# Performance work log

Hardware: AMD Instinct MI355X
Metric: run time of the kernel (lower is better)

Reference implementation:

```python
import jax, jax.numpy as jnp
import numpy as np

EPS = 1e-5  # BatchNorm eps (torch default)


def _coords():
    # coord_tensor[i] = [(i//5 - 2)/2, (i%5 - 2)/2] for 5x5 grid of 25 objects
    i = jnp.arange(25)
    return jnp.stack([(i // 5 - 2) / 2.0, (i % 5 - 2) / 2.0], axis=-1).astype(jnp.float32)


def _conv_bn(x, w, b, gamma, beta):
    # conv stride2 pad1 -> relu -> batchnorm (training-mode batch stats, as torch module default)
    y = jax.lax.conv_general_dilated(x, w, (2, 2), ((1, 1), (1, 1)),
                                     dimension_numbers=('NCHW', 'OIHW', 'NCHW'))
    y = jax.nn.relu(y + b[None, :, None, None])
    m = y.mean(axis=(0, 2, 3), keepdims=True)
    v = y.var(axis=(0, 2, 3), keepdims=True)
    return gamma[None, :, None, None] * (y - m) * jax.lax.rsqrt(v + EPS) + beta[None, :, None, None]


def setup_inputs() -> dict:
    key = jax.random.key(0)
    ks = iter(jax.random.split(key, 64))
    def rn(shape, scale=0.05):
        return jax.random.normal(next(ks), shape, jnp.float32) * scale
    B = 256
    inp = {
        'x': jax.random.normal(next(ks), (B, 3, 80, 80), jnp.float32),
        'qst': jax.random.normal(next(ks), (B, 11), jnp.float32),
    }
    for l, (ci, co) in enumerate([(3, 24), (24, 24), (24, 24), (24, 24)], 1):
        inp[f'cw{l}'] = rn((co, ci, 3, 3))
        inp[f'cb{l}'] = jnp.zeros((co,), jnp.float32)
        inp[f'bg{l}'] = jnp.ones((co,), jnp.float32)
        inp[f'bb{l}'] = jnp.zeros((co,), jnp.float32)
    for l, (di, do) in enumerate([(63, 256), (256, 256), (256, 256), (256, 256)], 1):
        inp[f'gw{l}'] = rn((di, do))
        inp[f'gb{l}'] = jnp.zeros((do,), jnp.float32)
    for l, (di, do) in enumerate([(256, 256), (256, 256), (256, 10)], 1):
        inp[f'fw{l}'] = rn((di, do))
        inp[f'fb{l}'] = jnp.zeros((do,), jnp.float32)
    return inp


def _forward(x, qst, cw1, cb1, bg1, bb1, cw2, cb2, bg2, bb2,
             cw3, cb3, bg3, bb3, cw4, cb4, bg4, bb4,
             gw1, gb1, gw2, gb2, gw3, gb3, gw4, gb4,
             fw1, fb1, fw2, fb2, fw3, fb3):
    B = x.shape[0]
    # Convolution stack: (B,3,80,80) -> (B,24,5,5)
    h = _conv_bn(x, cw1, cb1, bg1, bb1)
    h = _conv_bn(h, cw2, cb2, bg2, bb2)
    h = _conv_bn(h, cw3, cb3, bg3, bb3)
    h = _conv_bn(h, cw4, cb4, bg4, bb4)
    # Objects: (B,24,25) -> (B,25,24) -> concat coords -> (B,25,26)
    obj = h.reshape(B, 24, 25).transpose(0, 2, 1)
    obj = jnp.concatenate([obj, jnp.broadcast_to(_coords()[None], (B, 25, 2))], axis=-1)
    # Pairwise broadcast-concat: cat([x_i, x_j, qst]) with x_i[b,p,q]=obj[b,q], x_j[b,p,q]=obj[b,p]
    xi = jnp.broadcast_to(obj[:, None, :, :], (B, 25, 25, 26))
    xj = jnp.broadcast_to(obj[:, :, None, :], (B, 25, 25, 26))
    qb = jnp.broadcast_to(qst[:, None, None, :], (B, 25, 25, 11))
    pairs = jnp.concatenate([xi, xj, qb], axis=-1).reshape(B, 625, 63)
    g = jax.nn.relu(pairs @ gw1 + gb1)
    g = jax.nn.relu(g @ gw2 + gb2)
    g = jax.nn.relu(g @ gw3 + gb3)
    g = jax.nn.relu(g @ gw4 + gb4).sum(axis=1)  # (B,256)
    # f_phi (dropout treated as identity for a deterministic reference)
    f = jax.nn.relu(g @ fw1 + fb1)
    f = jax.nn.relu(f @ fw2 + fb2)
    logits = f @ fw3 + fb3
    return jax.nn.log_softmax(logits, axis=1)


def reference(x, qst, cw1, cb1, bg1, bb1, cw2, cb2, bg2, bb2,
              cw3, cb3, bg3, bb3, cw4, cb4, bg4, bb4,
              gw1, gb1, gw2, gb2, gw3, gb3, gw4, gb4,
              fw1, fb1, fw2, fb2, fw3, fb3):
    return _forward(x, qst, cw1, cb1, bg1, bb1, cw2, cb2, bg2, bb2,
                    cw3, cb3, bg3, bb3, cw4, cb4, bg4, bb4,
                    gw1, gb1, gw2, gb2, gw3, gb3, gw4, gb4,
                    fw1, fb1, fw2, fb2, fw3, fb3)
```

## Files before the change

### kernel.cpp

```cpp
#include <hip/hip_runtime.h>
#include <hip/hip_bf16.h>


typedef __attribute__((ext_vector_type(8))) short short8;
typedef __attribute__((ext_vector_type(4))) float floatx4;

__device__ __forceinline__ unsigned short f2bf(float v){
  union { float f; unsigned int u; } c; c.f = v;
  unsigned int u = c.u;
  u += 0x7FFFu + ((u >> 16) & 1u);
  return (unsigned short)(u >> 16);
}

__global__ __launch_bounds__(256) void prep_w_zero(
    const float* __restrict__ gw2, const float* __restrict__ gw3,
    const float* __restrict__ gw4, unsigned short* __restrict__ wf,
    float* __restrict__ stats)
{
  const int bid = blockIdx.x, tid = threadIdx.x;
  if (bid == 0){ for (int j = tid; j < 1536; j += 256) stats[j] = 0.f; }
  const int w = bid >> 8;
  const float* gw = (w == 0) ? gw2 : (w == 1) ? gw3 : gw4;
  const int idx = (bid & 255)*256 + tid;
  const int i = idx & 7, lane = (idx >> 3) & 63, t = (idx >> 9) & 15, kk = idx >> 13;
  const int k = kk*32 + (lane >> 4)*8 + i;
  const int c = t*16 + (lane & 15);
  wf[w*65536 + idx] = f2bf(gw[k*256 + c]);
}

template<int CI, int COG>
__global__ __launch_bounds__(256) void conv_relu_stats(
    const float* __restrict__ in,
    const float* __restrict__ stats_in, const float* __restrict__ gprev,
    const float* __restrict__ bprev, float invN,
    const float* __restrict__ cw, const float* __restrict__ cb,
    float* __restrict__ out, float* __restrict__ stats_out,
    int H, int W, int OH, int OW)
{
  const int co0 = blockIdx.y * COG;
  __shared__ float ssm[2*CI];
  __shared__ float psum[4][COG], psum2[4][COG];
  const int tid = threadIdx.x;
  if (tid < CI){
    if (stats_in){
      float S = 0.f, S2 = 0.f;
      #pragma unroll
      for (int sh = 0; sh < 8; sh++){ S += stats_in[sh*48 + tid]; S2 += stats_in[sh*48 + 24 + tid]; }
      const float mean = S*invN;
      const float var  = S2*invN - mean*mean;
      const float rs   = rsqrtf(var + 1e-5f);
      const float sc   = gprev[tid]*rs;
      ssm[tid] = sc; ssm[CI + tid] = bprev[tid] - mean*sc;
    } else { ssm[tid] = 1.f; ssm[CI + tid] = 0.f; }
  }
  __syncthreads();
  const int idx = blockIdx.x*256 + tid;
  const int ow = idx % OW; const int t2 = idx / OW;
  const int oh = t2 % OH;  const int b  = t2 / OH;
  const float* cwb = cw + co0*CI*9;
  float accv[COG];
  #pragma unroll
  for (int g = 0; g < COG; g++) accv[g] = cb[co0 + g];
  for (int ci = 0; ci < CI; ci++){
    const float* ip = in + ((long)(b*CI + ci))*H*W;
    const float sc = ssm[ci], sh2 = ssm[CI + ci];
    #pragma unroll
    for (int kh = 0; kh < 3; kh++){
      const int ih = oh*2 - 1 + kh;
      if ((unsigned)ih >= (unsigned)H) continue;
      #pragma unroll
      for (int kw = 0; kw < 3; kw++){
        const int iw = ow*2 - 1 + kw;
        if ((unsigned)iw >= (unsigned)W) continue;
        const float v = ip[ih*W + iw]*sc + sh2;
        #pragma unroll
        for (int g = 0; g < COG; g++)
          accv[g] += v * cwb[(g*CI + ci)*9 + kh*3 + kw];
      }
    }
  }
  const int wave = tid >> 6, lane = tid & 63;
  #pragma unroll
  for (int g = 0; g < COG; g++){
    const float v = fmaxf(accv[g], 0.f);
    accv[g] = v;
    out[(((long)b*24 + co0 + g)*OH + oh)*OW + ow] = v;
  }
  #pragma unroll
  for (int g = 0; g < COG; g++){
    float s = accv[g], s2 = accv[g]*accv[g];
    for (int off = 32; off; off >>= 1){ s += __shfl_down(s, off); s2 += __shfl_down(s2, off); }
    if (lane == 0){ psum[wave][g] = s; psum2[wave][g] = s2; }
  }
  __syncthreads();
  if (tid < COG){
    const float S  = psum[0][tid] + psum[1][tid] + psum[2][tid] + psum[3][tid];
    const float S2 = psum2[0][tid] + psum2[1][tid] + psum2[2][tid] + psum2[3][tid];
    const int sh = blockIdx.x & 7;
    atomicAdd(&stats_out[sh*48 + co0 + tid],      S);
    atomicAdd(&stats_out[sh*48 + 24 + co0 + tid], S2);
  }
}

__global__ __launch_bounds__(256) void build_ABQ(
    const float* __restrict__ y4, const float* __restrict__ stats4,
    const float* __restrict__ bg4, const float* __restrict__ bb4,
    const float* __restrict__ qst, const float* __restrict__ gw1,
    const float* __restrict__ gb1,
    float* __restrict__ A, float* __restrict__ Bm, float* __restrict__ Qv)
{
  const int b = blockIdx.x, tid = threadIdx.x;
  __shared__ float ssm[48];
  __shared__ float obj[25][26];
  if (tid < 24){
    float S = 0.f, S2 = 0.f;
    #pragma unroll
    for (int sh = 0; sh < 8; sh++){ S += stats4[sh*48 + tid]; S2 += stats4[sh*48 + 24 + tid]; }
    const float mean = S*(1.f/6400.f);
    const float var  = S2*(1.f/6400.f) - mean*mean;
    const float rs   = rsqrtf(var + 1e-5f);
    const float sc   = bg4[tid]*rs;
    ssm[tid] = sc; ssm[24 + tid] = bb4[tid] - mean*sc;
  }
  __syncthreads();
  for (int j = tid; j < 600; j += 256){
    const int q = j/24, c = j%24;
    obj[q][c] = ssm[c]*y4[((long)(b*24 + c))*25 + q] + ssm[24 + c];
  }
  if (tid < 50){
    const int q = tid >> 1;
    obj[q][24 + (tid & 1)] = (tid & 1) ? (float)(q%5 - 2)*0.5f : (float)(q/5 - 2)*0.5f;
  }
  __syncthreads();
  const int n = tid;
  float wa[26], wb[26];
  #pragma unroll
  for (int c = 0; c < 26; c++){ wa[c] = gw1[c*256 + n]; wb[c] = gw1[(26 + c)*256 + n]; }
  float qv = gb1[n];
  #pragma unroll
  for (int j = 0; j < 11; j++) qv += qst[b*11 + j]*gw1[(52 + j)*256 + n];
  Qv[b*256 + n] = qv;
  for (int q = 0; q < 25; q++){
    float a = 0.f, bm = 0.f;
    #pragma unroll
    for (int c = 0; c < 26; c++){ const float o = obj[q][c]; a += o*wa[c]; bm += o*wb[c]; }
    A [((long)(b*25 + q))*256 + n] = a;
    Bm[((long)(b*25 + q))*256 + n] = bm;
  }
}

__global__ __launch_bounds__(512) void g_fused(
    const float* __restrict__ A, const float* __restrict__ Bm, const float* __restrict__ Qv,
    const unsigned short* __restrict__ Wf,
    const float* __restrict__ gb2, const float* __restrict__ gb3, const float* __restrict__ gb4,
    float* __restrict__ gpart)
{
  __shared__ __align__(16) short act[128*256];
  __shared__ float scratch[512];
  const int tid = threadIdx.x;
  const int bidx = blockIdx.x;
  const int b = bidx / 5, blk = bidx % 5;
  const int rowbase = blk * 128;
  const int nrows = min(128, 625 - rowbase);
  char* actB = (char*)act;
  const int wave = tid >> 6, lane = tid & 63;
  const int lmod = lane & 15, ldiv = lane >> 4;
  const int wm = wave >> 2, wn = wave & 3;

  {
    const int r  = tid >> 2;
    const int q4 = tid & 3;
    if (r < nrows){
      const int row = rowbase + r;
      const float* ap = A  + ((long)(b*25 + row % 25))*256 + q4*4;
      const float* bp = Bm + ((long)(b*25 + row / 25))*256 + q4*4;
      const float* qp = Qv + b*256 + q4*4;
      #pragma unroll
      for (int j = 0; j < 16; j++){
        const int c = j*16;
        floatx4 av = *(const floatx4*)(ap + c);
        floatx4 bv = *(const floatx4*)(bp + c);
        floatx4 qv = *(const floatx4*)(qp + c);
        unsigned int p0 = (unsigned int)f2bf(fmaxf(av.x+bv.x+qv.x, 0.f))
                        | ((unsigned int)f2bf(fmaxf(av.y+bv.y+qv.y, 0.f)) << 16);
        unsigned int p1 = (unsigned int)f2bf(fmaxf(av.z+bv.z+qv.z, 0.f))
                        | ((unsigned int)f2bf(fmaxf(av.w+bv.w+qv.w, 0.f)) << 16);
        const int byte = (r*512 + (c + q4*4)*2) ^ ((r & 7) << 4);
        *(uint2*)(actB + byte) = make_uint2(p0, p1);
      }
    } else {
      #pragma unroll
      for (int j = 0; j < 16; j++){
        const int byte = (r*512 + (j*16 + q4*4)*2) ^ ((r & 7) << 4);
        *(uint2*)(actB + byte) = make_uint2(0u, 0u);
      }
    }
  }
  __syncthreads();

  for (int L = 0; L < 3; L++){
    floatx4 acc[4][4];
    #pragma unroll
    for (int m = 0; m < 4; m++)
      #pragma unroll
      for (int n = 0; n < 4; n++)
        acc[m][n] = (floatx4){0.f,0.f,0.f,0.f};
    const short8* wlayer = (const short8*)Wf + (long)L*8192;
    #pragma unroll
    for (int kk = 0; kk < 8; kk++){
      short8 bf[4];
      #pragma unroll
      for (int n = 0; n < 4; n++)
        bf[n] = wlayer[(kk*16 + wn*4 + n)*64 + lane];
      short8 af[4];
      #pragma unroll
      for (int m = 0; m < 4; m++){
        const int arow  = wm*64 + m*16 + lmod;
        const int abyte = (arow*512 + kk*64 + ldiv*16) ^ ((arow & 7) << 4);
        af[m] = *(const short8*)(actB + abyte);
      }
      #pragma unroll
      for (int n = 0; n < 4; n++)
        #pragma unroll
        for (int m = 0; m < 4; m++)
          acc[m][n] = __builtin_amdgcn_mfma_f32_16x16x32_bf16(af[m], bf[n], acc[m][n], 0, 0, 0);
    }

    if (L < 2){
      const float* bias = (L == 0) ? gb2 : gb3;
      __syncthreads();
      #pragma unroll
      for (int n = 0; n < 4; n++){
        const int c = (wn*4 + n)*16 + lmod;
        const float bv = bias[c];
        #pragma unroll
        for (int m = 0; m < 4; m++){
          #pragma unroll
          for (int i = 0; i < 4; i++){
            const int row = wm*64 + m*16 + ldiv*4 + i;
            const float v = fmaxf(acc[m][n][i] + bv, 0.f);
            const int byte = (row*512 + c*2) ^ ((row & 7) << 4);
            *(short*)(actB + byte) = (short)f2bf(v);
          }
        }
      }
      __syncthreads();
    } else {
      #pragma unroll
      for (int n = 0; n < 4; n++){
        const int c = (wn*4 + n)*16 + lmod;
        const float bv = gb4[c];
        float sv = 0.f;
        #pragma unroll
        for (int m = 0; m < 4; m++){
          #pragma unroll
          for (int i = 0; i < 4; i++){
            const int row = wm*64 + m*16 + ldiv*4 + i;
            const float v = fmaxf(acc[m][n][i] + bv, 0.f);
            if (row < nrows) sv += v;
          }
        }
        sv += __shfl_xor(sv, 16);
        sv += __shfl_xor(sv, 32);
        if (ldiv == 0) scratch[wm*256 + c] = sv;
      }
      __syncthreads();
      if (tid < 256) gpart[(long)bidx*256 + tid] = scratch[tid] + scratch[256 + tid];
    }
  }
}

__global__ __launch_bounds__(256) void f_phi(
    const float* __restrict__ gpart,
    const float* __restrict__ fw1, const float* __restrict__ fb1,
    const float* __restrict__ fw2, const float* __restrict__ fb2,
    const float* __restrict__ fw3, const float* __restrict__ fb3,
    float* __restrict__ out)
{
  const int b = blockIdx.x, n = threadIdx.x;
  __shared__ __align__(16) float bufA[256], bufB[256];
  __shared__ float lg[10];
  float g = 0.f;
  #pragma unroll
  for (int j = 0; j < 5; j++) g += gpart[((long)(b*5 + j))*256 + n];
  bufA[n] = g;
  __syncthreads();
  float acc = fb1[n];
  {
    const float4* pa = (const float4*)bufA;
    #pragma unroll 8
    for (int k4 = 0; k4 < 64; k4++){
      const float4 a = pa[k4];
      acc += a.x*fw1[(k4*4 + 0)*256 + n];
      acc += a.y*fw1[(k4*4 + 1)*256 + n];
      acc += a.z*fw1[(k4*4 + 2)*256 + n];
      acc += a.w*fw1[(k4*4 + 3)*256 + n];
    }
  }
  bufB[n] = fmaxf(acc, 0.f);
  __syncthreads();
  acc = fb2[n];
  {
    const float4* pb = (const float4*)bufB;
    #pragma unroll 8
    for (int k4 = 0; k4 < 64; k4++){
      const float4 a = pb[k4];
      acc += a.x*fw2[(k4*4 + 0)*256 + n];
      acc += a.y*fw2[(k4*4 + 1)*256 + n];
      acc += a.z*fw2[(k4*4 + 2)*256 + n];
      acc += a.w*fw2[(k4*4 + 3)*256 + n];
    }
  }
  __syncthreads();
  bufA[n] = fmaxf(acc, 0.f);
  __syncthreads();
  if (n < 10){
    float a3 = fb3[n];
    for (int k = 0; k < 256; k++) a3 += bufA[k]*fw3[k*10 + n];
    lg[n] = a3;
  }
  __syncthreads();
  if (n < 10){
    float m = lg[0];
    #pragma unroll
    for (int j = 1; j < 10; j++) m = fmaxf(m, lg[j]);
    float s = 0.f;
    #pragma unroll
    for (int j = 0; j < 10; j++) s += expf(lg[j] - m);
    out[b*10 + n] = lg[n] - m - logf(s);
  }
}

extern "C" void kernel_launch(void* const* d_in, const int* in_sizes, int n_in,
                              void* d_out, int out_size, void* d_ws, size_t ws_size,
                              hipStream_t stream)
{
  const float* x   = (const float*)d_in[0];
  const float* qst = (const float*)d_in[1];
  const float* cw1 = (const float*)d_in[2];
  const float* cb1 = (const float*)d_in[3];
  const float* bg1 = (const float*)d_in[4];
  const float* bb1 = (const float*)d_in[5];
  const float* cw2 = (const float*)d_in[6];
  const float* cb2 = (const float*)d_in[7];
  const float* bg2 = (const float*)d_in[8];
  const float* bb2 = (const float*)d_in[9];
  const float* cw3 = (const float*)d_in[10];
  const float* cb3 = (const float*)d_in[11];
  const float* bg3 = (const float*)d_in[12];
  const float* bb3 = (const float*)d_in[13];
  const float* cw4 = (const float*)d_in[14];
  const float* cb4 = (const float*)d_in[15];
  const float* bg4 = (const float*)d_in[16];
  const float* bb4 = (const float*)d_in[17];
  const float* gw1 = (const float*)d_in[18];
  const float* gb1 = (const float*)d_in[19];
  const float* gw2 = (const float*)d_in[20];
  const float* gb2 = (const float*)d_in[21];
  const float* gw3 = (const float*)d_in[22];
  const float* gb3 = (const float*)d_in[23];
  const float* gw4 = (const float*)d_in[24];
  const float* gb4 = (const float*)d_in[25];
  const float* fw1 = (const float*)d_in[26];
  const float* fb1 = (const float*)d_in[27];
  const float* fw2 = (const float*)d_in[28];
  const float* fb2 = (const float*)d_in[29];
  const float* fw3 = (const float*)d_in[30];
  const float* fb3 = (const float*)d_in[31];

  float* wsf    = (float*)d_ws;
  float* Qv     = wsf + 192;
  unsigned short* Wf = (unsigned short*)(wsf + 65728);
  float* stats  = wsf + 164032;
  float* y1     = wsf + 240832;
  float* Abuf   = y1;
  float* Bmbuf  = y1 + 1638400;
  float* y2     = wsf + 10071232;
  float* gpart  = y2;
  float* y3     = wsf + 12528832;
  float* y4     = wsf + 13143232;

  prep_w_zero<<<768, 256, 0, stream>>>(gw2, gw3, gw4, Wf, stats);
  conv_relu_stats<3,24><<<dim3(1600,1), 256, 0, stream>>>(x, nullptr, nullptr, nullptr, 0.f,
                                               cw1, cb1, y1, stats + 0, 80,80,40,40);
  conv_relu_stats<24,8><<<dim3(400,3), 256, 0, stream>>>(y1, stats + 0, bg1, bb1, 1.f/409600.f,
                                               cw2, cb2, y2, stats + 384, 40,40,20,20);
  conv_relu_stats<24,8><<<dim3(100,3), 256, 0, stream>>>(y2, stats + 384, bg2, bb2, 1.f/102400.f,
                                               cw3, cb3, y3, stats + 768, 20,20,10,10);
  conv_relu_stats<24,8><<<dim3(25,3), 256, 0, stream>>>(y3, stats + 768, bg3, bb3, 1.f/25600.f,
                                              cw4, cb4, y4, stats + 1152, 10,10,5,5);
  build_ABQ<<<256, 256, 0, stream>>>(y4, stats + 1152, bg4, bb4, qst, gw1, gb1,
                                     Abuf, Bmbuf, Qv);
  g_fused<<<1280, 512, 0, stream>>>(Abuf, Bmbuf, Qv, Wf, gb2, gb3, gb4, gpart);
  f_phi<<<256, 256, 0, stream>>>(gpart, fw1, fb1, fw2, fb2, fw3, fb3, (float*)d_out);
}
```

Baseline: 311.1 us.

## Fuse weight prep with conv1 and compute two outputs per thread in conv2/3

Merges the bf16 weight-swizzle kernel and the first convolution into one launch, with block ranges selecting the job, and moves the stats zeroing to a memset. Conv layers 2 and 3 now use a specialized kernel where each thread computes two adjacent output columns. The two outputs share a 5-wide input window, and their results are written as float2 stores. This cuts one kernel launch and reduces redundant input loads and index math, but adds per-thread register pressure and halves the grid size for those layers.

Measured after the change: 344.3 us. 1.11x slower.

```diff
diff --git a/kernel.cpp b/kernel.cpp
--- a/kernel.cpp
+++ b/kernel.cpp
@@ -12,20 +12,149 @@
   return (unsigned short)(u >> 16);
 }
 
-__global__ __launch_bounds__(256) void prep_w_zero(
+__global__ __launch_bounds__(256) void prep_conv1(
     const float* __restrict__ gw2, const float* __restrict__ gw3,
     const float* __restrict__ gw4, unsigned short* __restrict__ wf,
-    float* __restrict__ stats)
+    const float* __restrict__ x, const float* __restrict__ cw, const float* __restrict__ cb,
+    float* __restrict__ out, float* __restrict__ stats_out)
 {
   const int bid = blockIdx.x, tid = threadIdx.x;
-  if (bid == 0){ for (int j = tid; j < 1536; j += 256) stats[j] = 0.f; }
-  const int w = bid >> 8;
-  const float* gw = (w == 0) ? gw2 : (w == 1) ? gw3 : gw4;
-  const int idx = (bid & 255)*256 + tid;
-  const int i = idx & 7, lane = (idx >> 3) & 63, t = (idx >> 9) & 15, kk = idx >> 13;
-  const int k = kk*32 + (lane >> 4)*8 + i;
-  const int c = t*16 + (lane & 15);
-  wf[w*65536 + idx] = f2bf(gw[k*256 + c]);
+  if (bid < 768){
+    const int w = bid >> 8;
+    const float* gw = (w == 0) ? gw2 : (w == 1) ? gw3 : gw4;
+    const int idx = (bid & 255)*256 + tid;
+    const int i = idx & 7, lane = (idx >> 3) & 63, t = (idx >> 9) & 15, kk = idx >> 13;
+    const int k = kk*32 + (lane >> 4)*8 + i;
+    const int c = t*16 + (lane & 15);
+    wf[w*65536 + idx] = f2bf(gw[k*256 + c]);
+    return;
+  }
+  __shared__ float psum[4][24], psum2[4][24];
+  const int cbid = bid - 768;
+  const int idx = cbid*256 + tid;
+  const int ow = idx % 40; const int t2 = idx / 40;
+  const int oh = t2 % 40;  const int b  = t2 / 40 / 40 * 0 + idx / 1600;
+  float accv[24];
+  #pragma unroll
+  for (int g = 0; g < 24; g++) accv[g] = cb[g];
+  for (int ci = 0; ci < 3; ci++){
+    const float* ip = x + ((long)(b*3 + ci))*6400;
+    #pragma unroll
+    for (int kh = 0; kh < 3; kh++){
+      const int ih = oh*2 - 1 + kh;
+      if ((unsigned)ih >= 80u) continue;
+      #pragma unroll
+      for (int kw = 0; kw < 3; kw++){
+        const int iw = ow*2 - 1 + kw;
+        if ((unsigned)iw >= 80u) continue;
+        const float v = ip[ih*80 + iw];
+        #pragma unroll
+        for (int g = 0; g < 24; g++)
+          accv[g] += v * cw[(g*3 + ci)*9 + kh*3 + kw];
+      }
+    }
+  }
+  const int wave = tid >> 6, lane = tid & 63;
+  #pragma unroll
+  for (int g = 0; g < 24; g++){
+    const float v = fmaxf(accv[g], 0.f);
+    accv[g] = v;
+    out[(((long)b*24 + g)*40 + oh)*40 + ow] = v;
+  }
+  #pragma unroll
+  for (int g = 0; g < 24; g++){
+    float s = accv[g], s2 = accv[g]*accv[g];
+    for (int off = 32; off; off >>= 1){ s += __shfl_down(s, off); s2 += __shfl_down(s2, off); }
+    if (lane == 0){ psum[wave][g] = s; psum2[wave][g] = s2; }
+  }
+  __syncthreads();
+  if (tid < 24){
+    const float S  = psum[0][tid] + psum[1][tid] + psum[2][tid] + psum[3][tid];
+    const float S2 = psum2[0][tid] + psum2[1][tid] + psum2[2][tid] + psum2[3][tid];
+    const int sh = cbid & 7;
+    atomicAdd(&stats_out[sh*48 + tid],      S);
+    atomicAdd(&stats_out[sh*48 + 24 + tid], S2);
+  }
+}
+
+template<int OHt, int OWt, int Ht, int Wt>
+__global__ __launch_bounds__(256) void conv_pair8(
+    const float* __restrict__ in,
+    const float* __restrict__ stats_in, const float* __restrict__ gprev,
+    const float* __restrict__ bprev, float invN,
+    const float* __restrict__ cw, const float* __restrict__ cb,
+    float* __restrict__ out, float* __restrict__ stats_out)
+{
+  const int co0 = blockIdx.y * 8;
+  __shared__ float ssm[48];
+  __shared__ float psum[4][8], psum2[4][8];
+  const int tid = threadIdx.x;
+  if (tid < 24){
+    float S = 0.f, S2 = 0.f;
+    #pragma unroll
+    for (int sh = 0; sh < 8; sh++){ S += stats_in[sh*48 + tid]; S2 += stats_in[sh*48 + 24 + tid]; }
+    const float mean = S*invN;
+    const float var  = S2*invN - mean*mean;
+    const float rs   = rsqrtf(var + 1e-5f);
+    const float sc   = gprev[tid]*rs;
+    ssm[tid] = sc; ssm[24 + tid] = bprev[tid] - mean*sc;
+  }
+  __syncthreads();
+  constexpr int PPR = OWt/2;
+  const int idx = blockIdx.x*256 + tid;
+  const int pw = idx % PPR; const int t2 = idx / PPR;
+  const int oh = t2 % OHt;  const int b  = t2 / OHt;
+  const float* cwb = cw + co0*24*9;
+  float acc0[8], acc1[8];
+  #pragma unroll
+  for (int g = 0; g < 8; g++){ acc0[g] = cb[co0 + g]; acc1[g] = acc0[g]; }
+  for (int ci = 0; ci < 24; ci++){
+    const float* ip = in + ((long)(b*24 + ci))*Ht*Wt;
+    const float sc = ssm[ci], sh2 = ssm[24 + ci];
+    #pragma unroll
+    for (int kh = 0; kh < 3; kh++){
+      const int ih = oh*2 - 1 + kh;
+      if ((unsigned)ih >= (unsigned)Ht) continue;
+      const float* iprow = ip + ih*Wt + pw*4 - 1;
+      float v[5];
+      #pragma unroll
+      for (int t = 0; t < 5; t++){
+        const int iw = pw*4 - 1 + t;
+        v[t] = ((unsigned)iw < (unsigned)Wt) ? iprow[t]*sc + sh2 : 0.f;
+      }
+      #pragma unroll
+      for (int g = 0; g < 8; g++){
+        const float w0 = cwb[(g*24 + ci)*9 + kh*3 + 0];
+        const float w1 = cwb[(g*24 + ci)*9 + kh*3 + 1];
+        const float w2 = cwb[(g*24 + ci)*9 + kh*3 + 2];
+        acc0[g] += v[0]*w0 + v[1]*w1 + v[2]*w2;
+        acc1[g] += v[2]*w0 + v[3]*w1 + v[4]*w2;
+      }
+    }
+  }
+  const int wave = tid >> 6, lane = tid & 63;
+  #pragma unroll
+  for (int g = 0; g < 8; g++){
+    const float r0 = fmaxf(acc0[g], 0.f), r1 = fmaxf(acc1[g], 0.f);
+    acc0[g] = r0; acc1[g] = r1;
+    const long base = (((long)b*24 + co0 + g)*OHt + oh)*OWt + pw*2;
+    *(float2*)&out[base] = make_float2(r0, r1);
+  }
+  #pragma unroll
+  for (int g = 0; g < 8; g++){
+    float s = acc0[g] + acc1[g];
+    float s2 = acc0[g]*acc0[g] + acc1[g]*acc1[g];
+    for (int off = 32; off; off >>= 1){ s += __shfl_down(s, off); s2 += __shfl_down(s2, off); }
+    if (lane == 0){ psum[wave][g] = s; psum2[wave][g] = s2; }
+  }
+  __syncthreads();
+  if (tid < 8){
+    const float S  = psum[0][tid] + psum[1][tid] + psum[2][tid] + psum[3][tid];
+    const float S2 = psum2[0][tid] + psum2[1][tid] + psum2[2][tid] + psum2[3][tid];
+    const int sh = blockIdx.x & 7;
+    atomicAdd(&stats_out[sh*48 + co0 + tid],      S);
+    atomicAdd(&stats_out[sh*48 + 24 + co0 + tid], S2);
+  }
 }
 
 template<int CI, int COG>
@@ -42,16 +171,14 @@
   __shared__ float psum[4][COG], psum2[4][COG];
   const int tid = threadIdx.x;
   if (tid < CI){
-    if (stats_in){
-      float S = 0.f, S2 = 0.f;
-      #pragma unroll
-      for (int sh = 0; sh < 8; sh++){ S += stats_in[sh*48 + tid]; S2 += stats_in[sh*48 + 24 + tid]; }
-      const float mean = S*invN;
-      const float var  = S2*invN - mean*mean;
-      const float rs   = rsqrtf(var + 1e-5f);
-      const float sc   = gprev[tid]*rs;
-      ssm[tid] = sc; ssm[CI + tid] = bprev[tid] - mean*sc;
-    } else { ssm[tid] = 1.f; ssm[CI + tid] = 0.f; }
+    float S = 0.f, S2 = 0.f;
+    #pragma unroll
+    for (int sh = 0; sh < 8; sh++){ S += stats_in[sh*48 + tid]; S2 += stats_in[sh*48 + 24 + tid]; }
+    const float mean = S*invN;
+    const float var  = S2*invN - mean*mean;
+    const float rs   = rsqrtf(var + 1e-5f);
+    const float sc   = gprev[tid]*rs;
+    ssm[tid] = sc; ssm[CI + tid] = bprev[tid] - mean*sc;
   }
   __syncthreads();
   const int idx = blockIdx.x*256 + tid;
@@ -380,13 +507,12 @@
   float* y3     = wsf + 12528832;
   float* y4     = wsf + 13143232;
 
-  prep_w_zero<<<768, 256, 0, stream>>>(gw2, gw3, gw4, Wf, stats);
-  conv_relu_stats<3,24><<<dim3(1600,1), 256, 0, stream>>>(x, nullptr, nullptr, nullptr, 0.f,
-                                               cw1, cb1, y1, stats + 0, 80,80,40,40);
-  conv_relu_stats<24,8><<<dim3(400,3), 256, 0, stream>>>(y1, stats + 0, bg1, bb1, 1.f/409600.f,
-                                               cw2, cb2, y2, stats + 384, 40,40,20,20);
-  conv_relu_stats<24,8><<<dim3(100,3), 256, 0, stream>>>(y2, stats + 384, bg2, bb2, 1.f/102400.f,
-                                               cw3, cb3, y3, stats + 768, 20,20,10,10);
+  hipMemsetAsync(stats, 0, 1536*sizeof(float), stream);
+  prep_conv1<<<2368, 256, 0, stream>>>(gw2, gw3, gw4, Wf, x, cw1, cb1, y1, stats + 0);
+  conv_pair8<20,20,40,40><<<dim3(200,3), 256, 0, stream>>>(y1, stats + 0, bg1, bb1, 1.f/409600.f,
+                                               cw2, cb2, y2, stats + 384);
+  conv_pair8<10,10,20,20><<<dim3(50,3), 256, 0, stream>>>(y2, stats + 384, bg2, bb2, 1.f/102400.f,
+                                               cw3, cb3, y3, stats + 768);
   conv_relu_stats<24,8><<<dim3(25,3), 256, 0, stream>>>(y3, stats + 768, bg3, bb3, 1.f/25600.f,
                                               cw4, cb4, y4, stats + 1152, 10,10,5,5);
   build_ABQ<<<256, 256, 0, stream>>>(y4, stats + 1152, bg4, bb4, qst, gw1, gb1,
```

## Fuse pair-projection, g_theta MLP and f_phi head into one per-batch kernel

Applied to the files above, without the earlier changes.

Merges build_ABQ, g_fused and f_phi into a single kernel with one 512-thread block per batch element. The per-object A/B projections now stay in LDS, with Qv folded into A. The block loops over the five 128-row pair tiles and accumulates the pair sum in registers before running the f_phi MLP and log-softmax in place. This removes two kernel launches and the global writes and reads of A, Bm, Qv and the partial sums. In exchange the grid shrinks from 1280 blocks to 256, and each block needs roughly 120KB of LDS, which reduces occupancy and latency hiding on the MFMA phase.

New measurement: 293.0 us. -5.8%, faster.

```diff
diff --git a/kernel.cpp b/kernel.cpp
--- a/kernel.cpp
+++ b/kernel.cpp
@@ -102,16 +102,33 @@
   }
 }
 
-__global__ __launch_bounds__(256) void build_ABQ(
+__global__ __launch_bounds__(512) void g_mega(
     const float* __restrict__ y4, const float* __restrict__ stats4,
     const float* __restrict__ bg4, const float* __restrict__ bb4,
     const float* __restrict__ qst, const float* __restrict__ gw1,
     const float* __restrict__ gb1,
-    float* __restrict__ A, float* __restrict__ Bm, float* __restrict__ Qv)
+    const unsigned short* __restrict__ Wf,
+    const float* __restrict__ gb2, const float* __restrict__ gb3, const float* __restrict__ gb4,
+    const float* __restrict__ fw1, const float* __restrict__ fb1,
+    const float* __restrict__ fw2, const float* __restrict__ fb2,
+    const float* __restrict__ fw3, const float* __restrict__ fb3,
+    float* __restrict__ out)
 {
+  __shared__ __align__(16) short act[128*256];
+  __shared__ __align__(16) float A_lds[25][260];
+  __shared__ __align__(16) float Bm_lds[25][260];
+  __shared__ float obj[25][26];
+  __shared__ float ssm[48];
+  __shared__ float scratch[512];
+  __shared__ __align__(16) float bufA[256], bufB[256];
+  __shared__ float lg[10];
+
   const int b = blockIdx.x, tid = threadIdx.x;
-  __shared__ float ssm[48];
-  __shared__ float obj[25][26];
+  char* actB = (char*)act;
+  const int wave = tid >> 6, lane = tid & 63;
+  const int lmod = lane & 15, ldiv = lane >> 4;
+  const int wm = wave >> 2, wn = wave & 3;
+
   if (tid < 24){
     float S = 0.f, S2 = 0.f;
     #pragma unroll
@@ -123,7 +140,7 @@
     ssm[tid] = sc; ssm[24 + tid] = bb4[tid] - mean*sc;
   }
   __syncthreads();
-  for (int j = tid; j < 600; j += 256){
+  for (int j = tid; j < 600; j += 512){
     const int q = j/24, c = j%24;
     obj[q][c] = ssm[c]*y4[((long)(b*24 + c))*25 + q] + ssm[24 + c];
   }
@@ -132,161 +149,136 @@
     obj[q][24 + (tid & 1)] = (tid & 1) ? (float)(q%5 - 2)*0.5f : (float)(q/5 - 2)*0.5f;
   }
   __syncthreads();
-  const int n = tid;
-  float wa[26], wb[26];
-  #pragma unroll
-  for (int c = 0; c < 26; c++){ wa[c] = gw1[c*256 + n]; wb[c] = gw1[(26 + c)*256 + n]; }
-  float qv = gb1[n];
-  #pragma unroll
-  for (int j = 0; j < 11; j++) qv += qst[b*11 + j]*gw1[(52 + j)*256 + n];
-  Qv[b*256 + n] = qv;
-  for (int q = 0; q < 25; q++){
-    float a = 0.f, bm = 0.f;
-    #pragma unroll
-    for (int c = 0; c < 26; c++){ const float o = obj[q][c]; a += o*wa[c]; bm += o*wb[c]; }
-    A [((long)(b*25 + q))*256 + n] = a;
-    Bm[((long)(b*25 + q))*256 + n] = bm;
-  }
-}
-
-__global__ __launch_bounds__(512) void g_fused(
-    const float* __restrict__ A, const float* __restrict__ Bm, const float* __restrict__ Qv,
-    const unsigned short* __restrict__ Wf,
-    const float* __restrict__ gb2, const float* __restrict__ gb3, const float* __restrict__ gb4,
-    float* __restrict__ gpart)
-{
-  __shared__ __align__(16) short act[128*256];
-  __shared__ float scratch[512];
-  const int tid = threadIdx.x;
-  const int bidx = blockIdx.x;
-  const int b = bidx / 5, blk = bidx % 5;
-  const int rowbase = blk * 128;
-  const int nrows = min(128, 625 - rowbase);
-  char* actB = (char*)act;
-  const int wave = tid >> 6, lane = tid & 63;
-  const int lmod = lane & 15, ldiv = lane >> 4;
-  const int wm = wave >> 2, wn = wave & 3;
-
   {
-    const int r  = tid >> 2;
-    const int q4 = tid & 3;
-    if (r < nrows){
-      const int row = rowbase + r;
-      const float* ap = A  + ((long)(b*25 + row % 25))*256 + q4*4;
-      const float* bp = Bm + ((long)(b*25 + row / 25))*256 + q4*4;
-      const float* qp = Qv + b*256 + q4*4;
-      #pragma unroll
-      for (int j = 0; j < 16; j++){
-        const int c = j*16;
-        floatx4 av = *(const floatx4*)(ap + c);
-        floatx4 bv = *(const floatx4*)(bp + c);
-        floatx4 qv = *(const floatx4*)(qp + c);
-        unsigned int p0 = (unsigned int)f2bf(fmaxf(av.x+bv.x+qv.x, 0.f))
-                        | ((unsigned int)f2bf(fmaxf(av.y+bv.y+qv.y, 0.f)) << 16);
-        unsigned int p1 = (unsigned int)f2bf(fmaxf(av.z+bv.z+qv.z, 0.f))
-                        | ((unsigned int)f2bf(fmaxf(av.w+bv.w+qv.w, 0.f)) << 16);
-        const int byte = (r*512 + (c + q4*4)*2) ^ ((r & 7) << 4);
-        *(uint2*)(actB + byte) = make_uint2(p0, p1);
+    const int n = tid & 255, half = tid >> 8;
+    float wa[26], wb[26];
+    #pragma unroll
+    for (int c = 0; c < 26; c++){ wa[c] = gw1[c*256 + n]; wb[c] = gw1[(26 + c)*256 + n]; }
+    float qv = gb1[n];
+    #pragma unroll
+    for (int j = 0; j < 11; j++) qv += qst[b*11 + j]*gw1[(52 + j)*256 + n];
+    const int q0 = half ? 13 : 0, q1 = half ? 25 : 13;
+    for (int q = q0; q < q1; q++){
+      float a = qv, bm = 0.f;
+      #pragma unroll
+      for (int c = 0; c < 26; c++){ const float o = obj[q][c]; a += o*wa[c]; bm += o*wb[c]; }
+      A_lds[q][n] = a; Bm_lds[q][n] = bm;
+    }
+  }
+  __syncthreads();
+
+  float gsum = 0.f;
+  for (int blk = 0; blk < 5; blk++){
+    const int rowbase = blk * 128;
+    const int nrows = min(128, 625 - rowbase);
+    {
+      const int r  = tid >> 2;
+      const int q4 = tid & 3;
+      if (r < nrows){
+        const int row = rowbase + r;
+        const float* ap = &A_lds [row % 25][q4*4];
+        const float* bp = &Bm_lds[row / 25][q4*4];
+        #pragma unroll
+        for (int j = 0; j < 16; j++){
+          const int c = j*16;
+          floatx4 av = *(const floatx4*)(ap + c);
+          floatx4 bv = *(const floatx4*)(bp + c);
+          unsigned int p0 = (unsigned int)f2bf(fmaxf(av.x+bv.x, 0.f))
+                          | ((unsigned int)f2bf(fmaxf(av.y+bv.y, 0.f)) << 16);
+          unsigned int p1 = (unsigned int)f2bf(fmaxf(av.z+bv.z, 0.f))
+                          | ((unsigned int)f2bf(fmaxf(av.w+bv.w, 0.f)) << 16);
+          const int byte = (r*512 + (c + q4*4)*2) ^ ((r & 7) << 4);
+          *(uint2*)(actB + byte) = make_uint2(p0, p1);
+        }
+      } else {
+        #pragma unroll
+        for (int j = 0; j < 16; j++){
+          const int byte = (r*512 + (j*16 + q4*4)*2) ^ ((r & 7) << 4);
+          *(uint2*)(actB + byte) = make_uint2(0u, 0u);
+        }
       }
-    } else {
-      #pragma unroll
-      for (int j = 0; j < 16; j++){
-        const int byte = (r*512 + (j*16 + q4*4)*2) ^ ((r & 7) << 4);
-        *(uint2*)(actB + byte) = make_uint2(0u, 0u);
+    }
+    __syncthreads();
+
+    for (int L = 0; L < 3; L++){
+      floatx4 acc[4][4];
+      #pragma unroll
+      for (int m = 0; m < 4; m++)
+        #pragma unroll
+        for (int n = 0; n < 4; n++)
+          acc[m][n] = (floatx4){0.f,0.f,0.f,0.f};
+      const short8* wlayer = (const short8*)Wf + (long)L*8192;
+      #pragma unroll
+      for (int kk = 0; kk < 8; kk++){
+        short8 bf[4];
+        #pragma unroll
+        for (int n = 0; n < 4; n++)
+          bf[n] = wlayer[(kk*16 + wn*4 + n)*64 + lane];
+        short8 af[4];
+        #pragma unroll
+        for (int m = 0; m < 4; m++){
+          const int arow  = wm*64 + m*16 + lmod;
+          const int abyte = (arow*512 + kk*64 + ldiv*16) ^ ((arow & 7) << 4);
+          af[m] = *(const short8*)(actB + abyte);
+        }
+        #pragma unroll
+        for (int n = 0; n < 4; n++)
+          #pragma unroll
+          for (int m = 0; m < 4; m++)
+            acc[m][n] = __builtin_amdgcn_mfma_f32_16x16x32_bf16(af[m], bf[n], acc[m][n], 0, 0, 0);
       }
-    }
-  }
-  __syncthreads();
-
-  for (int L = 0; L < 3; L++){
-    floatx4 acc[4][4];
-    #pragma unroll
-    for (int m = 0; m < 4; m++)
-      #pragma unroll
-      for (int n = 0; n < 4; n++)
-        acc[m][n] = (floatx4){0.f,0.f,0.f,0.f};
-    const short8* wlayer = (const short8*)Wf + (long)L*8192;
-    #pragma unroll
-    for (int kk = 0; kk < 8; kk++){
-      short8 bf[4];
-      #pragma unroll
-      for (int n = 0; n < 4; n++)
-        bf[n] = wlayer[(kk*16 + wn*4 + n)*64 + lane];
-      short8 af[4];
-      #pragma unroll
-      for (int m = 0; m < 4; m++){
-        const int arow  = wm*64 + m*16 + lmod;
-        const int abyte = (arow*512 + kk*64 + ldiv*16) ^ ((arow & 7) << 4);
-        af[m] = *(const short8*)(actB + abyte);
+
+      if (L < 2){
+        const float* bias = (L == 0) ? gb2 : gb3;
+        __syncthreads();
+        #pragma unroll
+        for (int n = 0; n < 4; n++){
+          const int c = (wn*4 + n)*16 + lmod;
+          const float bv = bias[c];
+          #pragma unroll
+          for (int m = 0; m < 4; m++){
+            #pragma unroll
+            for (int i = 0; i < 4; i++){
+              const int row = wm*64 + m*16 + ldiv*4 + i;
+              const float v = fmaxf(acc[m][n][i] + bv, 0.f);
+              const int byte = (row*512 + c*2) ^ ((row & 7) << 4);
+              *(short*)(actB + byte) = (short)f2bf(v);
+            }
+          }
+        }
+        __syncthreads();
+      } else {
+        __syncthreads();
+        #pragma unroll
+        for (int n = 0; n < 4; n++){
+          const int c = (wn*4 + n)*16 + lmod;
+          const float bv = gb4[c];
+          float sv = 0.f;
+          #pragma unroll
+          for (int m = 0; m < 4; m++){
+            #pragma unroll
+            for (int i = 0; i < 4; i++){
+              const int row = wm*64 + m*16 + ldiv*4 + i;
+              const float v = fmaxf(acc[m][n][i] + bv, 0.f);
+              if (row < nrows) sv += v;
+            }
+          }
+          sv += __shfl_xor(sv, 16);
+          sv += __shfl_xor(sv, 32);
+          if (ldiv == 0) scratch[wm*256 + c] = sv;
+        }
+        __syncthreads();
+        if (tid < 256) gsum += scratch[tid] + scratch[256 + tid];
       }
-      #pragma unroll
-      for (int n = 0; n < 4; n++)
-        #pragma unroll
-        for (int m = 0; m < 4; m++)
-          acc[m][n] = __builtin_amdgcn_mfma_f32_16x16x32_bf16(af[m], bf[n], acc[m][n], 0, 0, 0);
-    }
-
-    if (L < 2){
-      const float* bias = (L == 0) ? gb2 : gb3;
-      __syncthreads();
-      #pragma unroll
-      for (int n = 0; n < 4; n++){
-        const int c = (wn*4 + n)*16 + lmod;
-        const float bv = bias[c];
-        #pragma unroll
-        for (int m = 0; m < 4; m++){
-          #pragma unroll
-          for (int i = 0; i < 4; i++){
-            const int row = wm*64 + m*16 + ldiv*4 + i;
-            const float v = fmaxf(acc[m][n][i] + bv, 0.f);
-            const int byte = (row*512 + c*2) ^ ((row & 7) << 4);
-            *(short*)(actB + byte) = (short)f2bf(v);
-          }
-        }
-      }
-      __syncthreads();
-    } else {
-      #pragma unroll
-      for (int n = 0; n < 4; n++){
-        const int c = (wn*4 + n)*16 + lmod;
-        const float bv = gb4[c];
-        float sv = 0.f;
-        #pragma unroll
-        for (int m = 0; m < 4; m++){
-          #pragma unroll
-          for (int i = 0; i < 4; i++){
-            const int row = wm*64 + m*16 + ldiv*4 + i;
-            const float v = fmaxf(acc[m][n][i] + bv, 0.f);
-            if (row < nrows) sv += v;
-          }
-        }
-        sv += __shfl_xor(sv, 16);
-        sv += __shfl_xor(sv, 32);
-        if (ldiv == 0) scratch[wm*256 + c] = sv;
-      }
-      __syncthreads();
-      if (tid < 256) gpart[(long)bidx*256 + tid] = scratch[tid] + scratch[256 + tid];
-    }
-  }
-}
-
-__global__ __launch_bounds__(256) void f_phi(
-    const float* __restrict__ gpart,
-    const float* __restrict__ fw1, const float* __restrict__ fb1,
-    const float* __restrict__ fw2, const float* __restrict__ fb2,
-    const float* __restrict__ fw3, const float* __restrict__ fb3,
-    float* __restrict__ out)
-{
-  const int b = blockIdx.x, n = threadIdx.x;
-  __shared__ __align__(16) float bufA[256], bufB[256];
-  __shared__ float lg[10];
-  float g = 0.f;
-  #pragma unroll
-  for (int j = 0; j < 5; j++) g += gpart[((long)(b*5 + j))*256 + n];
-  bufA[n] = g;
-  __syncthreads();
-  float acc = fb1[n];
-  {
+    }
+  }
+
+  if (tid < 256) bufA[tid] = gsum;
+  __syncthreads();
+  const int n = tid & 255;
+  float acc = 0.f;
+  if (tid < 256){
+    acc = fb1[n];
     const float4* pa = (const float4*)bufA;
     #pragma unroll 8
     for (int k4 = 0; k4 < 64; k4++){
@@ -296,11 +288,11 @@
       acc += a.z*fw1[(k4*4 + 2)*256 + n];
       acc += a.w*fw1[(k4*4 + 3)*256 + n];
     }
-  }
-  bufB[n] = fmaxf(acc, 0.f);
-  __syncthreads();
-  acc = fb2[n];
-  {
+    bufB[n] = fmaxf(acc, 0.f);
+  }
+  __syncthreads();
+  if (tid < 256){
+    acc = fb2[n];
     const float4* pb = (const float4*)bufB;
     #pragma unroll 8
     for (int k4 = 0; k4 < 64; k4++){
@@ -312,22 +304,22 @@
     }
   }
   __syncthreads();
-  bufA[n] = fmaxf(acc, 0.f);
-  __syncthreads();
-  if (n < 10){
-    float a3 = fb3[n];
-    for (int k = 0; k < 256; k++) a3 += bufA[k]*fw3[k*10 + n];
-    lg[n] = a3;
-  }
-  __syncthreads();
-  if (n < 10){
+  if (tid < 256) bufA[n] = fmaxf(acc, 0.f);
+  __syncthreads();
+  if (tid < 10){
+    float a3 = fb3[tid];
+    for (int k = 0; k < 256; k++) a3 += bufA[k]*fw3[k*10 + tid];
+    lg[tid] = a3;
+  }
+  __syncthreads();
+  if (tid < 10){
     float m = lg[0];
     #pragma unroll
     for (int j = 1; j < 10; j++) m = fmaxf(m, lg[j]);
     float s = 0.f;
     #pragma unroll
     for (int j = 0; j < 10; j++) s += expf(lg[j] - m);
-    out[b*10 + n] = lg[n] - m - logf(s);
+    out[b*10 + tid] = lg[tid] - m - logf(s);
   }
 }
 
@@ -369,14 +361,10 @@
   const float* fb3 = (const float*)d_in[31];
 
   float* wsf    = (float*)d_ws;
-  float* Qv     = wsf + 192;
   unsigned short* Wf = (unsigned short*)(wsf + 65728);
   float* stats  = wsf + 164032;
   float* y1     = wsf + 240832;
-  float* Abuf   = y1;
-  float* Bmbuf  = y1 + 1638400;
   float* y2     = wsf + 10071232;
-  float* gpart  = y2;
   float* y3     = wsf + 12528832;
   float* y4     = wsf + 13143232;
 
@@ -389,8 +377,7 @@
                                                cw3, cb3, y3, stats + 768, 20,20,10,10);
   conv_relu_stats<24,8><<<dim3(25,3), 256, 0, stream>>>(y3, stats + 768, bg3, bb3, 1.f/25600.f,
                                               cw4, cb4, y4, stats + 1152, 10,10,5,5);
-  build_ABQ<<<256, 256, 0, stream>>>(y4, stats + 1152, bg4, bb4, qst, gw1, gb1,
-                                     Abuf, Bmbuf, Qv);
-  g_fused<<<1280, 512, 0, stream>>>(Abuf, Bmbuf, Qv, Wf, gb2, gb3, gb4, gpart);
-  f_phi<<<256, 256, 0, stream>>>(gpart, fw1, fb1, fw2, fb2, fw3, fb3, (float*)d_out);
-}
+  g_mega<<<256, 512, 0, stream>>>(y4, stats + 1152, bg4, bb4, qst, gw1, gb1, Wf,
+                                  gb2, gb3, gb4, fw1, fb1, fw2, fb2, fw3, fb3,
+                                  (float*)d_out);
+}
```
